# Optimization experiments

Hardware: AMD Instinct MI355X
Metric: run time of the kernel (lower is better)

## Reference

```python
import jax, jax.numpy as jnp
import numpy as np

N = 50000          # nodes
E_RAND = 800000    # random edges (avg degree 16)
IN, HID, HEADS, OUT = 256, 64, 4, 40
NEG_SLOPE = 0.2    # PyG GATConv default leaky_relu slope
BN_EPS = 1e-5


def setup_inputs() -> dict:
    key = jax.random.key(0)
    ks = jax.random.split(key, 24)
    x = jax.random.normal(ks[0], (N, IN), jnp.float32)
    ei = jax.random.randint(ks[1], (2, E_RAND), 0, N)
    loops = jnp.arange(N, dtype=ei.dtype)
    edge_index = jnp.concatenate([ei, jnp.stack([loops, loops])], axis=1)  # add self loops (PyG default)
    s = 0.1
    d = {
        "x": x,
        "edge_index": edge_index,
        "W0": jax.random.normal(ks[2], (IN, HEADS * HID), jnp.float32) * s,
        "a_src0": jax.random.normal(ks[3], (HEADS, HID), jnp.float32) * s,
        "a_dst0": jax.random.normal(ks[4], (HEADS, HID), jnp.float32) * s,
        "b0": jax.random.normal(ks[5], (HEADS * HID,), jnp.float32) * s,
        "bn0_g": jnp.ones((HEADS * HID,), jnp.float32),
        "bn0_b": jnp.zeros((HEADS * HID,), jnp.float32),
        "bn0_m": jax.random.normal(ks[6], (HEADS * HID,), jnp.float32) * s,
        "bn0_v": jax.random.uniform(ks[7], (HEADS * HID,), jnp.float32, 0.5, 1.5),
        "W1": jax.random.normal(ks[8], (HEADS * HID, HEADS * HID), jnp.float32) * s,
        "a_src1": jax.random.normal(ks[9], (HEADS, HID), jnp.float32) * s,
        "a_dst1": jax.random.normal(ks[10], (HEADS, HID), jnp.float32) * s,
        "b1": jax.random.normal(ks[11], (HEADS * HID,), jnp.float32) * s,
        "bn1_g": jnp.ones((HEADS * HID,), jnp.float32),
        "bn1_b": jnp.zeros((HEADS * HID,), jnp.float32),
        "bn1_m": jax.random.normal(ks[12], (HEADS * HID,), jnp.float32) * s,
        "bn1_v": jax.random.uniform(ks[13], (HEADS * HID,), jnp.float32, 0.5, 1.5),
        "W2": jax.random.normal(ks[14], (HEADS * HID, OUT), jnp.float32) * s,
        "a_src2": jax.random.normal(ks[15], (1, OUT), jnp.float32) * s,
        "a_dst2": jax.random.normal(ks[16], (1, OUT), jnp.float32) * s,
        "b2": jax.random.normal(ks[17], (OUT,), jnp.float32) * s,
    }
    return d


def gat_conv(x, edge_index, W, att_src, att_dst, heads, ch):
    """PyG GATConv (eval mode): gather -> leaky_relu attn -> segment softmax -> scatter add."""
    src, dst = edge_index[0], edge_index[1]
    h = (x @ W).reshape(-1, heads, ch)                       # [N,H,C]
    a_s = jnp.einsum('nhc,hc->nh', h, att_src)
    a_d = jnp.einsum('nhc,hc->nh', h, att_dst)
    e = jax.nn.leaky_relu(a_s[src] + a_d[dst], NEG_SLOPE)    # [E,H]
    m = jax.ops.segment_max(e, dst, num_segments=N)
    m = jax.lax.stop_gradient(jnp.where(jnp.isfinite(m), m, 0.0))
    p = jnp.exp(e - m[dst])
    denom = jax.ops.segment_sum(p, dst, num_segments=N)
    alpha = p / (denom[dst] + 1e-16)                         # [E,H]
    msg = h[src] * alpha[:, :, None]                         # [E,H,C]
    return jax.ops.segment_sum(msg, dst, num_segments=N)     # [N,H,C]


def _bn(h, g, b, m, v):
    return g * (h - m) * jax.lax.rsqrt(v + BN_EPS) + b


def reference(x, edge_index, W0, a_src0, a_dst0, b0, bn0_g, bn0_b, bn0_m, bn0_v,
              W1, a_src1, a_dst1, b1, bn1_g, bn1_b, bn1_m, bn1_v,
              W2, a_src2, a_dst2, b2):
    h = gat_conv(x, edge_index, W0, a_src0, a_dst0, HEADS, HID).reshape(N, HEADS * HID) + b0
    h = jax.nn.elu(_bn(h, bn0_g, bn0_b, bn0_m, bn0_v))
    h = gat_conv(h, edge_index, W1, a_src1, a_dst1, HEADS, HID).reshape(N, HEADS * HID) + b1
    h = jax.nn.elu(_bn(h, bn1_g, bn1_b, bn1_m, bn1_v))
    out = gat_conv(h, edge_index, W2, a_src2, a_dst2, 1, OUT).reshape(N, OUT) + b2
    return out
```

## Files before the change

### kernel.cpp

```cpp
#include <hip/hip_runtime.h>
#include <cstdint>
#include <cstddef>

constexpr int kN = 50000;
constexpr float kSlope = 0.2f;
constexpr float kBnEps = 1e-5f;

static inline int ceil_div(int a, int b) { return (a + b - 1) / b; }

typedef __attribute__((ext_vector_type(8))) _Float16 half8;
typedef __attribute__((ext_vector_type(8))) unsigned short ushortx8;
typedef __attribute__((ext_vector_type(4))) float f32x4;

__device__ inline unsigned short f2h_us(float f) {
  _Float16 h = (_Float16)f;
  return *(unsigned short*)&h;
}

__device__ inline void gload16(const void* g, void* l) {
  __builtin_amdgcn_global_load_lds((const __attribute__((address_space(1))) unsigned int*)g,
                                   (__attribute__((address_space(3))) unsigned int*)l, 16, 0, 0);
}


__global__ void k_degree(const int* __restrict__ dst, int* __restrict__ deg, int E) {
  int e = blockIdx.x * blockDim.x + threadIdx.x;
  if (e < E) atomicAdd(&deg[dst[e]], 1);
}

__global__ void k_scan1(const int* __restrict__ deg, int* __restrict__ rp,
                        int* __restrict__ bsum, int n) {
  __shared__ int sm[256];
  int i = blockIdx.x * 256 + threadIdx.x;
  int v = (i < n) ? deg[i] : 0;
  sm[threadIdx.x] = v;
  __syncthreads();
  for (int off = 1; off < 256; off <<= 1) {
    int t = (threadIdx.x >= off) ? sm[threadIdx.x - off] : 0;
    __syncthreads();
    sm[threadIdx.x] += t;
    __syncthreads();
  }
  if (i < n) rp[i + 1] = sm[threadIdx.x];
  if (threadIdx.x == 255) bsum[blockIdx.x] = sm[255];
}

__global__ void k_scan2(int* bsum, int nb) {
  __shared__ int sm[256];
  int v = (threadIdx.x < nb) ? bsum[threadIdx.x] : 0;
  sm[threadIdx.x] = v;
  __syncthreads();
  for (int off = 1; off < 256; off <<= 1) {
    int t = (threadIdx.x >= off) ? sm[threadIdx.x - off] : 0;
    __syncthreads();
    sm[threadIdx.x] += t;
    __syncthreads();
  }
  if (threadIdx.x < nb) bsum[threadIdx.x] = sm[threadIdx.x] - v;
}

__global__ void k_scan3(int* __restrict__ rp, const int* __restrict__ bsum, int n) {
  int i = blockIdx.x * 256 + threadIdx.x;
  if (i < n) rp[i + 1] += bsum[blockIdx.x];
  if (i == 0) rp[0] = 0;
}

__global__ void k_scatter(const int* __restrict__ src, const int* __restrict__ dst,
                          const int* __restrict__ rp, int* __restrict__ cur,
                          int* __restrict__ csr, int E) {
  int e = blockIdx.x * blockDim.x + threadIdx.x;
  if (e < E) {
    int d = dst[e];
    int pos = rp[d] + atomicAdd(&cur[d], 1);
    csr[pos] = src[e];
  }
}


__global__ void k_prep(const float* __restrict__ x, unsigned short* __restrict__ x16,
                       const float* __restrict__ W0, unsigned short* __restrict__ Wt0,
                       const float* __restrict__ W1, unsigned short* __restrict__ Wt1,
                       const float* __restrict__ W2, unsigned short* __restrict__ Wt2) {
  int i = blockIdx.x * blockDim.x + threadIdx.x;
  const int N4 = kN * 64;
  const int S0 = 256 * 256, S1 = 256 * 256, S2 = 128 * 256;
  if (i < N4) {
    float4 v = ((const float4*)x)[i];
    ushort4 o;
    o.x = f2h_us(v.x);
    o.y = f2h_us(v.y);
    o.z = f2h_us(v.z);
    o.w = f2h_us(v.w);
    ((ushort4*)x16)[i] = o;
  } else {
    int j = i - N4;
    if (j < S0) {
      int nc = j >> 8, k = j & 255;
      Wt0[j] = f2h_us(W0[(size_t)k * 256 + nc]);
    } else if (j < S0 + S1) {
      int t = j - S0;
      int nc = t >> 8, k = t & 255;
      Wt1[t] = f2h_us(W1[(size_t)k * 256 + nc]);
    } else if (j < S0 + S1 + S2) {
      int t = j - S0 - S1;
      int nc = t >> 8, k = t & 255;
      Wt2[t] = (nc < 40) ? f2h_us(W2[(size_t)k * 40 + nc]) : (unsigned short)0;
    }
  }
}


__global__ __launch_bounds__(256) void k_mfma_gemm(
    const unsigned short* __restrict__ A, const unsigned short* __restrict__ Bt,
    unsigned short* __restrict__ C, const float* __restrict__ asrc,
    const float* __restrict__ adst, float* __restrict__ a_s, float* __restrict__ a_d, int M,
    int K, int Nc, int ldc, int heads, int acols) {
  constexpr int BM = 128, BK = 32;
  __shared__ unsigned short As[BM * BK];
  __shared__ unsigned short Bs[BM * BK];
  int tid = threadIdx.x;
  int wave = tid >> 6, lane = tid & 63;
  int quad = lane >> 4, l16 = lane & 15;
  int wm = (wave & 1) * 64, wn = (wave >> 1) * 64;
  int bm = blockIdx.x * BM, bn = blockIdx.y * BM;
  int srow = lane >> 2;
  int spart = lane & 3;
  f32x4 acc[4][4] = {};
  for (int k0 = 0; k0 < K; k0 += BK) {
#pragma unroll
    for (int it = 0; it < 2; it++) {
      int chunk = wave * 2 + it;
      int row = chunk * 16 + srow;
      gload16(A + (size_t)(bm + row) * K + k0 + spart * 8, As + chunk * 512);
      gload16(Bt + (size_t)(bn + row) * K + k0 + spart * 8, Bs + chunk * 512);
    }
    __syncthreads();
    half8 af[4], bf[4];
#pragma unroll
    for (int i = 0; i < 4; i++) {
      af[i] = *(const half8*)(As + (wm + i * 16 + l16) * BK + quad * 8);
      bf[i] = *(const half8*)(Bs + (wn + i * 16 + l16) * BK + quad * 8);
    }
#pragma unroll
    for (int i = 0; i < 4; i++)
#pragma unroll
      for (int j = 0; j < 4; j++)
        acc[i][j] = __builtin_amdgcn_mfma_f32_16x16x32_f16(af[i], bf[j], acc[i][j], 0, 0, 0);
    __syncthreads();
  }
#pragma unroll
  for (int i = 0; i < 4; i++) {
#pragma unroll
    for (int j = 0; j < 4; j++) {
      int col = bn + wn + j * 16 + l16;
      if (col >= Nc) continue;
#pragma unroll
      for (int r = 0; r < 4; r++) {
        int row = bm + wm + i * 16 + quad * 4 + r;
        if (row < M) C[(size_t)row * ldc + col] = f2h_us(acc[i][j][r]);
      }
    }
  }
  int ghead = (bn + wn) >> 6;
  if (ghead < heads) {
    float asv[4], adv[4];
#pragma unroll
    for (int j = 0; j < 4; j++) {
      int col = bn + wn + j * 16 + l16;
      bool ok = col < acols;
      asv[j] = ok ? asrc[col] : 0.f;
      adv[j] = ok ? adst[col] : 0.f;
    }
#pragma unroll
    for (int i = 0; i < 4; i++) {
#pragma unroll
      for (int r = 0; r < 4; r++) {
        float s = acc[i][0][r] * asv[0] + acc[i][1][r] * asv[1] + acc[i][2][r] * asv[2] +
                  acc[i][3][r] * asv[3];
        float d = acc[i][0][r] * adv[0] + acc[i][1][r] * adv[1] + acc[i][2][r] * adv[2] +
                  acc[i][3][r] * adv[3];
#pragma unroll
        for (int mask = 1; mask <= 8; mask <<= 1) {
          s += __shfl_xor(s, mask, 64);
          d += __shfl_xor(d, mask, 64);
        }
        if (l16 == 0) {
          int row = bm + wm + i * 16 + quad * 4 + r;
          if (row < M) {
            a_s[row * heads + ghead] = s;
            a_d[row * heads + ghead] = d;
          }
        }
      }
    }
  }
}


__global__ __launch_bounds__(256) void k_attn_agg256(
    const int* __restrict__ rp, const int* __restrict__ csr, const _Float16* __restrict__ h,
    const float* __restrict__ a_s, const float* __restrict__ a_d, const float* __restrict__ bias,
    const float* __restrict__ bg, const float* __restrict__ bb, const float* __restrict__ bm,
    const float* __restrict__ bv, unsigned short* __restrict__ out, int n_nodes) {
  int wid = (blockIdx.x * blockDim.x + threadIdx.x) >> 6;
  int lane = threadIdx.x & 63;
  if (wid >= n_nodes) return;
  int n = wid;
  int beg = rp[n], end = rp[n + 1];
  int half = lane >> 5, l32 = lane & 31;
  int head = l32 >> 3;
  int c = l32 * 8;
  float ad = a_d[n * 4 + head];
  float acc[8] = {};
  float psum = 0.f;
  int e = beg;
  for (; e + 8 <= end; e += 8) {
    int s0 = csr[e + half];
    int s1 = csr[e + 2 + half];
    int s2 = csr[e + 4 + half];
    int s3 = csr[e + 6 + half];
    float x0 = a_s[s0 * 4 + head] + ad;
    float x1 = a_s[s1 * 4 + head] + ad;
    float x2 = a_s[s2 * 4 + head] + ad;
    float x3 = a_s[s3 * 4 + head] + ad;
    half8 v0 = *(const half8*)(h + (size_t)s0 * 256 + c);
    half8 v1 = *(const half8*)(h + (size_t)s1 * 256 + c);
    half8 v2 = *(const half8*)(h + (size_t)s2 * 256 + c);
    half8 v3 = *(const half8*)(h + (size_t)s3 * 256 + c);
    x0 = x0 > 0.f ? x0 : x0 * kSlope;
    x1 = x1 > 0.f ? x1 : x1 * kSlope;
    x2 = x2 > 0.f ? x2 : x2 * kSlope;
    x3 = x3 > 0.f ? x3 : x3 * kSlope;
    float p0 = __expf(x0), p1 = __expf(x1);
    float p2 = __expf(x2), p3 = __expf(x3);
    psum += (p0 + p1) + (p2 + p3);
#pragma unroll
    for (int j = 0; j < 8; j++) {
      acc[j] += (float)v0[j] * p0 + (float)v1[j] * p1;
      acc[j] += (float)v2[j] * p2 + (float)v3[j] * p3;
    }
  }
  for (; e + 2 <= end; e += 2) {
    int s0 = csr[e + half];
    float x0 = a_s[s0 * 4 + head] + ad;
    x0 = x0 > 0.f ? x0 : x0 * kSlope;
    float p0 = __expf(x0);
    psum += p0;
    half8 v0 = *(const half8*)(h + (size_t)s0 * 256 + c);
#pragma unroll
    for (int j = 0; j < 8; j++) acc[j] += (float)v0[j] * p0;
  }
  if (e < end && half == 0) {
    int s0 = csr[e];
    float x0 = a_s[s0 * 4 + head] + ad;
    x0 = x0 > 0.f ? x0 : x0 * kSlope;
    float p0 = __expf(x0);
    psum += p0;
    half8 v0 = *(const half8*)(h + (size_t)s0 * 256 + c);
#pragma unroll
    for (int j = 0; j < 8; j++) acc[j] += (float)v0[j] * p0;
  }
  psum += __shfl_xor(psum, 32, 64);
#pragma unroll
  for (int j = 0; j < 8; j++) acc[j] += __shfl_xor(acc[j], 32, 64);
  if (half == 0) {
    float rden = 1.f / (psum + 1e-16f);
    ushortx8 o;
#pragma unroll
    for (int j = 0; j < 8; j++) {
      float v = acc[j] * rden + bias[c + j];
      v = bg[c + j] * (v - bm[c + j]) * rsqrtf(bv[c + j] + kBnEps) + bb[c + j];
      v = v > 0.f ? v : (__expf(v) - 1.f);
      o[j] = f2h_us(v);
    }
    *(ushortx8*)(out + (size_t)n * 256 + c) = o;
  }
}


__global__ __launch_bounds__(256) void k_attn_agg40(
    const int* __restrict__ rp, const int* __restrict__ csr, const _Float16* __restrict__ h,
    const float* __restrict__ a_s, const float* __restrict__ a_d, const float* __restrict__ bias,
    float* __restrict__ out, int n_nodes) {
  int wid = (blockIdx.x * blockDim.x + threadIdx.x) >> 6;
  int lane = threadIdx.x & 63;
  if (wid >= n_nodes) return;
  int n = wid;
  int beg = rp[n], end = rp[n + 1];
  float ad = a_d[n];
  int grp = lane >> 3, l8 = lane & 7;
  int c = l8 * 8;
  bool act = l8 < 5;
  float acc[8] = {};
  float psum = 0.f;
  for (int base = beg; base < end; base += 16) {
    int e0 = base + grp;
    int e1 = base + 8 + grp;
    if (e0 < end) {
      int s = csr[e0];
      float x = a_s[s] + ad;
      x = x > 0.f ? x : x * kSlope;
      float p = __expf(x);
      psum += p;
      if (act) {
        half8 hv = *(const half8*)(h + (size_t)s * 40 + c);
#pragma unroll
        for (int j = 0; j < 8; j++) acc[j] += (float)hv[j] * p;
      }
    }
    if (e1 < end) {
      int s = csr[e1];
      float x = a_s[s] + ad;
      x = x > 0.f ? x : x * kSlope;
      float p = __expf(x);
      psum += p;
      if (act) {
        half8 hv = *(const half8*)(h + (size_t)s * 40 + c);
#pragma unroll
        for (int j = 0; j < 8; j++) acc[j] += (float)hv[j] * p;
      }
    }
  }
#pragma unroll
  for (int mask = 8; mask <= 32; mask <<= 1) psum += __shfl_xor(psum, mask, 64);
#pragma unroll
  for (int j = 0; j < 8; j++) {
#pragma unroll
    for (int mask = 8; mask <= 32; mask <<= 1) acc[j] += __shfl_xor(acc[j], mask, 64);
  }
  if (lane < 5) {
    float rden = 1.f / (psum + 1e-16f);
    float4 o0, o1;
    o0.x = acc[0] * rden + bias[c + 0];
    o0.y = acc[1] * rden + bias[c + 1];
    o0.z = acc[2] * rden + bias[c + 2];
    o0.w = acc[3] * rden + bias[c + 3];
    o1.x = acc[4] * rden + bias[c + 4];
    o1.y = acc[5] * rden + bias[c + 5];
    o1.z = acc[6] * rden + bias[c + 6];
    o1.w = acc[7] * rden + bias[c + 7];
    *(float4*)(out + (size_t)n * 40 + c) = o0;
    *(float4*)(out + (size_t)n * 40 + c + 4) = o1;
  }
}


extern "C" void kernel_launch(void* const* d_in, const int* in_sizes, int n_in, void* d_out,
                              int out_size, void* d_ws, size_t ws_size, hipStream_t stream) {
  const float* x = (const float*)d_in[0];
  const int* ei = (const int*)d_in[1];
  const float* W0 = (const float*)d_in[2];
  const float* as0 = (const float*)d_in[3];
  const float* ad0 = (const float*)d_in[4];
  const float* b0 = (const float*)d_in[5];
  const float* bg0 = (const float*)d_in[6];
  const float* bb0 = (const float*)d_in[7];
  const float* bm0 = (const float*)d_in[8];
  const float* bv0 = (const float*)d_in[9];
  const float* W1 = (const float*)d_in[10];
  const float* as1 = (const float*)d_in[11];
  const float* ad1 = (const float*)d_in[12];
  const float* b1 = (const float*)d_in[13];
  const float* bg1 = (const float*)d_in[14];
  const float* bb1 = (const float*)d_in[15];
  const float* bm1 = (const float*)d_in[16];
  const float* bv1 = (const float*)d_in[17];
  const float* W2 = (const float*)d_in[18];
  const float* as2 = (const float*)d_in[19];
  const float* ad2 = (const float*)d_in[20];
  const float* b2 = (const float*)d_in[21];
  float* out = (float*)d_out;

  const int E = in_sizes[1] / 2;
  const int* srcIdx = ei;
  const int* dstIdx = ei + E;

  char* p = (char*)d_ws;
  auto alloc = [&](size_t bytes) -> void* {
    void* r = (void*)p;
    p += (bytes + 255) & ~(size_t)255;
    return r;
  };
  int* rp = (int*)alloc((kN + 1) * sizeof(int));
  int* degcur = (int*)alloc((size_t)2 * kN * sizeof(int));
  int* deg = degcur;
  int* cur = degcur + kN;
  int* bsum = (int*)alloc(256 * sizeof(int));
  int* csr = (int*)alloc((size_t)E * sizeof(int));
  float* a_s = (float*)alloc((size_t)kN * 4 * sizeof(float));
  float* a_d = (float*)alloc((size_t)kN * 4 * sizeof(float));
  unsigned short* x16 = (unsigned short*)alloc((size_t)kN * 256 * 2);
  unsigned short* h16 = (unsigned short*)alloc((size_t)kN * 256 * 2);
  unsigned short* act16 = (unsigned short*)alloc((size_t)kN * 256 * 2);
  unsigned short* Wt0 = (unsigned short*)alloc((size_t)256 * 256 * 2);
  unsigned short* Wt1 = (unsigned short*)alloc((size_t)256 * 256 * 2);
  unsigned short* Wt2 = (unsigned short*)alloc((size_t)128 * 256 * 2);

  const int eb = ceil_div(E, 256);
  const int nb = ceil_div(kN, 256);

  hipMemsetAsync(degcur, 0, (size_t)2 * kN * sizeof(int), stream);
  k_degree<<<eb, 256, 0, stream>>>(dstIdx, deg, E);
  k_scan1<<<nb, 256, 0, stream>>>(deg, rp, bsum, kN);
  k_scan2<<<1, 256, 0, stream>>>(bsum, nb);
  k_scan3<<<nb, 256, 0, stream>>>(rp, bsum, kN);
  k_scatter<<<eb, 256, 0, stream>>>(srcIdx, dstIdx, rp, cur, csr, E);

  const int prep_items = kN * 64 + 256 * 256 * 2 + 128 * 256;
  k_prep<<<ceil_div(prep_items, 256), 256, 0, stream>>>(x, x16, W0, Wt0, W1, Wt1, W2, Wt2);

  dim3 gg(ceil_div(kN, 128), 2);
  dim3 gg2(ceil_div(kN, 128), 1);
  int wpn_blocks = ceil_div(kN, 4);

  k_mfma_gemm<<<gg, 256, 0, stream>>>(x16, Wt0, h16, as0, ad0, a_s, a_d, kN, 256, 256, 256, 4,
                                      256);
  k_attn_agg256<<<wpn_blocks, 256, 0, stream>>>(rp, csr, (const _Float16*)h16, a_s, a_d, b0, bg0,
                                                bb0, bm0, bv0, act16, kN);

  k_mfma_gemm<<<gg, 256, 0, stream>>>(act16, Wt1, h16, as1, ad1, a_s, a_d, kN, 256, 256, 256, 4,
                                      256);
  k_attn_agg256<<<wpn_blocks, 256, 0, stream>>>(rp, csr, (const _Float16*)h16, a_s, a_d, b1, bg1,
                                                bb1, bm1, bv1, act16, kN);

  k_mfma_gemm<<<gg2, 256, 0, stream>>>(act16, Wt2, h16, as2, ad2, a_s, a_d, kN, 256, 40, 40, 1,
                                       40);
  k_attn_agg40<<<wpn_blocks, 256, 0, stream>>>(rp, csr, (const _Float16*)h16, a_s, a_d, b2, out,
                                               kN);
}
```

Before: 459.1 us.

## Split 256-wide aggregation into two half-channel blocks with 4 edge lanes per wave

The 256-channel attention aggregation now assigns each node to two blocks, each covering 128 channels. Within a wave, four 16-lane groups each take a different edge, handling eight edges per iteration. The separate unrolled and remainder loops are replaced by one loop that clamps out-of-range edge indices and zeroes their weights. This doubles the number of waves and raises edge-level parallelism per wave, aiming to hide gather latency on low-degree nodes, at the cost of loading each edge's index and attention score twice and doing more cross-lane reduction.

Measured after the change: 472.1 us. 1.03x slower.

```diff
diff --git a/kernel.cpp b/kernel.cpp
--- a/kernel.cpp
+++ b/kernel.cpp
@@ -202,68 +202,47 @@
     const float* __restrict__ a_s, const float* __restrict__ a_d, const float* __restrict__ bias,
     const float* __restrict__ bg, const float* __restrict__ bb, const float* __restrict__ bm,
     const float* __restrict__ bv, unsigned short* __restrict__ out, int n_nodes) {
-  int wid = (blockIdx.x * blockDim.x + threadIdx.x) >> 6;
+  int hf = blockIdx.x & 1;
+  int wave = threadIdx.x >> 6;
   int lane = threadIdx.x & 63;
-  if (wid >= n_nodes) return;
-  int n = wid;
+  int n = (blockIdx.x >> 1) * 4 + wave;
+  if (n >= n_nodes) return;
   int beg = rp[n], end = rp[n + 1];
-  int half = lane >> 5, l32 = lane & 31;
-  int head = l32 >> 3;
-  int c = l32 * 8;
+  int q = lane >> 4, l16 = lane & 15;
+  int c = hf * 128 + l16 * 8;
+  int head = c >> 6;
   float ad = a_d[n * 4 + head];
   float acc[8] = {};
   float psum = 0.f;
-  int e = beg;
-  for (; e + 8 <= end; e += 8) {
-    int s0 = csr[e + half];
-    int s1 = csr[e + 2 + half];
-    int s2 = csr[e + 4 + half];
-    int s3 = csr[e + 6 + half];
-    float x0 = a_s[s0 * 4 + head] + ad;
-    float x1 = a_s[s1 * 4 + head] + ad;
-    float x2 = a_s[s2 * 4 + head] + ad;
-    float x3 = a_s[s3 * 4 + head] + ad;
-    half8 v0 = *(const half8*)(h + (size_t)s0 * 256 + c);
-    half8 v1 = *(const half8*)(h + (size_t)s1 * 256 + c);
-    half8 v2 = *(const half8*)(h + (size_t)s2 * 256 + c);
-    half8 v3 = *(const half8*)(h + (size_t)s3 * 256 + c);
-    x0 = x0 > 0.f ? x0 : x0 * kSlope;
-    x1 = x1 > 0.f ? x1 : x1 * kSlope;
-    x2 = x2 > 0.f ? x2 : x2 * kSlope;
-    x3 = x3 > 0.f ? x3 : x3 * kSlope;
-    float p0 = __expf(x0), p1 = __expf(x1);
-    float p2 = __expf(x2), p3 = __expf(x3);
-    psum += (p0 + p1) + (p2 + p3);
-#pragma unroll
-    for (int j = 0; j < 8; j++) {
-      acc[j] += (float)v0[j] * p0 + (float)v1[j] * p1;
-      acc[j] += (float)v2[j] * p2 + (float)v3[j] * p3;
-    }
-  }
-  for (; e + 2 <= end; e += 2) {
-    int s0 = csr[e + half];
-    float x0 = a_s[s0 * 4 + head] + ad;
-    x0 = x0 > 0.f ? x0 : x0 * kSlope;
-    float p0 = __expf(x0);
-    psum += p0;
-    half8 v0 = *(const half8*)(h + (size_t)s0 * 256 + c);
-#pragma unroll
-    for (int j = 0; j < 8; j++) acc[j] += (float)v0[j] * p0;
-  }
-  if (e < end && half == 0) {
-    int s0 = csr[e];
-    float x0 = a_s[s0 * 4 + head] + ad;
-    x0 = x0 > 0.f ? x0 : x0 * kSlope;
-    float p0 = __expf(x0);
-    psum += p0;
-    half8 v0 = *(const half8*)(h + (size_t)s0 * 256 + c);
-#pragma unroll
-    for (int j = 0; j < 8; j++) acc[j] += (float)v0[j] * p0;
-  }
+  int last = end - 1;
+  for (int e = beg; e < end; e += 8) {
+    int ea = e + q, eb = e + 4 + q;
+    int ia = (ea <= last) ? ea : last;
+    int ib = (eb <= last) ? eb : last;
+    int sa = csr[ia];
+    int sb = csr[ib];
+    float ta = a_s[sa * 4 + head];
+    float tb = a_s[sb * 4 + head];
+    half8 va = *(const half8*)(h + (size_t)sa * 256 + c);
+    half8 vb = *(const half8*)(h + (size_t)sb * 256 + c);
+    float xa = ta + ad, xb = tb + ad;
+    xa = xa > 0.f ? xa : xa * kSlope;
+    xb = xb > 0.f ? xb : xb * kSlope;
+    float pa = __expf(xa), pb = __expf(xb);
+    pa = (ea < end) ? pa : 0.f;
+    pb = (eb < end) ? pb : 0.f;
+    psum += pa + pb;
+#pragma unroll
+    for (int j = 0; j < 8; j++) acc[j] += (float)va[j] * pa + (float)vb[j] * pb;
+  }
+  psum += __shfl_xor(psum, 16, 64);
   psum += __shfl_xor(psum, 32, 64);
 #pragma unroll
-  for (int j = 0; j < 8; j++) acc[j] += __shfl_xor(acc[j], 32, 64);
-  if (half == 0) {
+  for (int j = 0; j < 8; j++) {
+    acc[j] += __shfl_xor(acc[j], 16, 64);
+    acc[j] += __shfl_xor(acc[j], 32, 64);
+  }
+  if (q == 0) {
     float rden = 1.f / (psum + 1e-16f);
     ushortx8 o;
 #pragma unroll
@@ -411,17 +390,18 @@
 
   dim3 gg(ceil_div(kN, 128), 2);
   dim3 gg2(ceil_div(kN, 128), 1);
+  int agg256_blocks = 2 * ceil_div(kN, 4);
   int wpn_blocks = ceil_div(kN, 4);
 
   k_mfma_gemm<<<gg, 256, 0, stream>>>(x16, Wt0, h16, as0, ad0, a_s, a_d, kN, 256, 256, 256, 4,
                                       256);
-  k_attn_agg256<<<wpn_blocks, 256, 0, stream>>>(rp, csr, (const _Float16*)h16, a_s, a_d, b0, bg0,
-                                                bb0, bm0, bv0, act16, kN);
+  k_attn_agg256<<<agg256_blocks, 256, 0, stream>>>(rp, csr, (const _Float16*)h16, a_s, a_d, b0,
+                                                   bg0, bb0, bm0, bv0, act16, kN);
 
   k_mfma_gemm<<<gg, 256, 0, stream>>>(act16, Wt1, h16, as1, ad1, a_s, a_d, kN, 256, 256, 256, 4,
                                       256);
-  k_attn_agg256<<<wpn_blocks, 256, 0, stream>>>(rp, csr, (const _Float16*)h16, a_s, a_d, b1, bg1,
-                                                bb1, bm1, bv1, act16, kN);
+  k_attn_agg256<<<agg256_blocks, 256, 0, stream>>>(rp, csr, (const _Float16*)h16, a_s, a_d, b1,
+                                                   bg1, bb1, bm1, bv1, act16, kN);
 
   k_mfma_gemm<<<gg2, 256, 0, stream>>>(act16, Wt2, h16, as2, ad2, a_s, a_d, kN, 256, 40, 40, 1,
                                        40);
```

## Fuse CSR build, scans and prep into one cooperative kernel

Applied to the files above, without the earlier changes.

Replaces the memset, degree count, three scan kernels, scatter and fp16 prep kernels with a single cooperative kernel of 1024 blocks that uses grid-wide syncs between phases. The aim is to remove several kernel launches and the gaps between them. In exchange each phase runs with a fixed grid-stride loop of limited parallelism, and five grid syncs are added, which may cost more than the launches they replace.

Result: slower. 993.5 us (+116.4%).

```diff
diff --git a/kernel.cpp b/kernel.cpp
--- a/kernel.cpp
+++ b/kernel.cpp
@@ -1,6 +1,9 @@
 #include <hip/hip_runtime.h>
+#include <hip/hip_cooperative_groups.h>
 #include <cstdint>
 #include <cstddef>
+
+namespace cg = cooperative_groups;
 
 constexpr int kN = 50000;
 constexpr float kSlope = 0.2f;
@@ -23,89 +26,100 @@
 }
 
 
-__global__ void k_degree(const int* __restrict__ dst, int* __restrict__ deg, int E) {
-  int e = blockIdx.x * blockDim.x + threadIdx.x;
-  if (e < E) atomicAdd(&deg[dst[e]], 1);
-}
-
-__global__ void k_scan1(const int* __restrict__ deg, int* __restrict__ rp,
-                        int* __restrict__ bsum, int n) {
+__global__ void k_build(const int* __restrict__ src, const int* __restrict__ dst,
+                        int* __restrict__ rp, int* __restrict__ deg, int* __restrict__ cur,
+                        int* __restrict__ bsum, int* __restrict__ csr, int E, int n,
+                        const float* __restrict__ x, unsigned short* __restrict__ x16,
+                        const float* __restrict__ W0, unsigned short* __restrict__ Wt0,
+                        const float* __restrict__ W1, unsigned short* __restrict__ Wt1,
+                        const float* __restrict__ W2, unsigned short* __restrict__ Wt2) {
+  cg::grid_group grid = cg::this_grid();
+  const int tid = blockIdx.x * blockDim.x + threadIdx.x;
+  const int nthr = gridDim.x * blockDim.x;
   __shared__ int sm[256];
-  int i = blockIdx.x * 256 + threadIdx.x;
-  int v = (i < n) ? deg[i] : 0;
-  sm[threadIdx.x] = v;
-  __syncthreads();
-  for (int off = 1; off < 256; off <<= 1) {
-    int t = (threadIdx.x >= off) ? sm[threadIdx.x - off] : 0;
+
+  for (int i = tid; i < n; i += nthr) {
+    deg[i] = 0;
+    cur[i] = 0;
+  }
+  {
+    const int N4 = kN * 64;
+    const int S0 = 256 * 256, S1 = 256 * 256, S2 = 128 * 256;
+    const int total = N4 + S0 + S1 + S2;
+    for (int i = tid; i < total; i += nthr) {
+      if (i < N4) {
+        float4 v = ((const float4*)x)[i];
+        ushort4 o;
+        o.x = f2h_us(v.x);
+        o.y = f2h_us(v.y);
+        o.z = f2h_us(v.z);
+        o.w = f2h_us(v.w);
+        ((ushort4*)x16)[i] = o;
+      } else {
+        int j = i - N4;
+        if (j < S0) {
+          int nc = j >> 8, k = j & 255;
+          Wt0[j] = f2h_us(W0[(size_t)k * 256 + nc]);
+        } else if (j < S0 + S1) {
+          int t = j - S0;
+          int nc = t >> 8, k = t & 255;
+          Wt1[t] = f2h_us(W1[(size_t)k * 256 + nc]);
+        } else {
+          int t = j - S0 - S1;
+          int nc = t >> 8, k = t & 255;
+          Wt2[t] = (nc < 40) ? f2h_us(W2[(size_t)k * 40 + nc]) : (unsigned short)0;
+        }
+      }
+    }
+  }
+  grid.sync();
+
+  for (int e = tid; e < E; e += nthr) atomicAdd(&deg[dst[e]], 1);
+  grid.sync();
+
+  const int nchunks = (n + 255) / 256;
+  for (int c = blockIdx.x; c < nchunks; c += gridDim.x) {
+    int i = c * 256 + threadIdx.x;
+    int v = (i < n) ? deg[i] : 0;
+    sm[threadIdx.x] = v;
     __syncthreads();
-    sm[threadIdx.x] += t;
+    for (int off = 1; off < 256; off <<= 1) {
+      int t = (threadIdx.x >= off) ? sm[threadIdx.x - off] : 0;
+      __syncthreads();
+      sm[threadIdx.x] += t;
+      __syncthreads();
+    }
+    if (i < n) rp[i + 1] = sm[threadIdx.x];
+    if (threadIdx.x == 255) bsum[c] = sm[255];
     __syncthreads();
   }
-  if (i < n) rp[i + 1] = sm[threadIdx.x];
-  if (threadIdx.x == 255) bsum[blockIdx.x] = sm[255];
-}
-
-__global__ void k_scan2(int* bsum, int nb) {
-  __shared__ int sm[256];
-  int v = (threadIdx.x < nb) ? bsum[threadIdx.x] : 0;
-  sm[threadIdx.x] = v;
-  __syncthreads();
-  for (int off = 1; off < 256; off <<= 1) {
-    int t = (threadIdx.x >= off) ? sm[threadIdx.x - off] : 0;
+  grid.sync();
+
+  if (blockIdx.x == 0) {
+    int v = (threadIdx.x < nchunks) ? bsum[threadIdx.x] : 0;
+    sm[threadIdx.x] = v;
     __syncthreads();
-    sm[threadIdx.x] += t;
-    __syncthreads();
-  }
-  if (threadIdx.x < nb) bsum[threadIdx.x] = sm[threadIdx.x] - v;
-}
-
-__global__ void k_scan3(int* __restrict__ rp, const int* __restrict__ bsum, int n) {
-  int i = blockIdx.x * 256 + threadIdx.x;
-  if (i < n) rp[i + 1] += bsum[blockIdx.x];
-  if (i == 0) rp[0] = 0;
-}
-
-__global__ void k_scatter(const int* __restrict__ src, const int* __restrict__ dst,
-                          const int* __restrict__ rp, int* __restrict__ cur,
-                          int* __restrict__ csr, int E) {
-  int e = blockIdx.x * blockDim.x + threadIdx.x;
-  if (e < E) {
+    for (int off = 1; off < 256; off <<= 1) {
+      int t = (threadIdx.x >= off) ? sm[threadIdx.x - off] : 0;
+      __syncthreads();
+      sm[threadIdx.x] += t;
+      __syncthreads();
+    }
+    if (threadIdx.x < nchunks) bsum[threadIdx.x] = sm[threadIdx.x] - v;
+  }
+  grid.sync();
+
+  for (int c = blockIdx.x; c < nchunks; c += gridDim.x) {
+    int i = c * 256 + threadIdx.x;
+    if (i < n) rp[i + 1] += bsum[c];
+  }
+  if (tid == 0) rp[0] = 0;
+  grid.sync();
+
+  for (int e = tid; e < E; e += nthr) {
     int d = dst[e];
     int pos = rp[d] + atomicAdd(&cur[d], 1);
     csr[pos] = src[e];
-  }
-}
-
-
-__global__ void k_prep(const float* __restrict__ x, unsigned short* __restrict__ x16,
-                       const float* __restrict__ W0, unsigned short* __restrict__ Wt0,
-                       const float* __restrict__ W1, unsigned short* __restrict__ Wt1,
-                       const float* __restrict__ W2, unsigned short* __restrict__ Wt2) {
-  int i = blockIdx.x * blockDim.x + threadIdx.x;
-  const int N4 = kN * 64;
-  const int S0 = 256 * 256, S1 = 256 * 256, S2 = 128 * 256;
-  if (i < N4) {
-    float4 v = ((const float4*)x)[i];
-    ushort4 o;
-    o.x = f2h_us(v.x);
-    o.y = f2h_us(v.y);
-    o.z = f2h_us(v.z);
-    o.w = f2h_us(v.w);
-    ((ushort4*)x16)[i] = o;
-  } else {
-    int j = i - N4;
-    if (j < S0) {
-      int nc = j >> 8, k = j & 255;
-      Wt0[j] = f2h_us(W0[(size_t)k * 256 + nc]);
-    } else if (j < S0 + S1) {
-      int t = j - S0;
-      int nc = t >> 8, k = t & 255;
-      Wt1[t] = f2h_us(W1[(size_t)k * 256 + nc]);
-    } else if (j < S0 + S1 + S2) {
-      int t = j - S0 - S1;
-      int nc = t >> 8, k = t & 255;
-      Wt2[t] = (nc < 40) ? f2h_us(W2[(size_t)k * 40 + nc]) : (unsigned short)0;
-    }
   }
 }
 
@@ -396,18 +410,14 @@
   unsigned short* Wt1 = (unsigned short*)alloc((size_t)256 * 256 * 2);
   unsigned short* Wt2 = (unsigned short*)alloc((size_t)128 * 256 * 2);
 
-  const int eb = ceil_div(E, 256);
-  const int nb = ceil_div(kN, 256);
-
-  hipMemsetAsync(degcur, 0, (size_t)2 * kN * sizeof(int), stream);
-  k_degree<<<eb, 256, 0, stream>>>(dstIdx, deg, E);
-  k_scan1<<<nb, 256, 0, stream>>>(deg, rp, bsum, kN);
-  k_scan2<<<1, 256, 0, stream>>>(bsum, nb);
-  k_scan3<<<nb, 256, 0, stream>>>(rp, bsum, kN);
-  k_scatter<<<eb, 256, 0, stream>>>(srcIdx, dstIdx, rp, cur, csr, E);
-
-  const int prep_items = kN * 64 + 256 * 256 * 2 + 128 * 256;
-  k_prep<<<ceil_div(prep_items, 256), 256, 0, stream>>>(x, x16, W0, Wt0, W1, Wt1, W2, Wt2);
+  {
+    int Ee = E, nn = kN;
+    void* args[] = {(void*)&srcIdx, (void*)&dstIdx, (void*)&rp,  (void*)&deg, (void*)&cur,
+                    (void*)&bsum,   (void*)&csr,    (void*)&Ee,  (void*)&nn,  (void*)&x,
+                    (void*)&x16,    (void*)&W0,     (void*)&Wt0, (void*)&W1,  (void*)&Wt1,
+                    (void*)&W2,     (void*)&Wt2};
+    hipLaunchCooperativeKernel((const void*)k_build, dim3(1024), dim3(256), args, 0, stream);
+  }
 
   dim3 gg(ceil_div(kN, 128), 2);
   dim3 gg2(ceil_div(kN, 128), 1);
```

## Fuse degree count with fp16 prep, and CSR scatter with first GEMM

Applied to the files above, without the earlier changes.

Merges the degree-counting kernel with the fp16 conversion/transpose prep into one grid-stride kernel. It also runs the CSR scatter as extra blocks of the layer-0 GEMM launch, since the two are independent. This removes two kernel launches and lets the atomic-heavy scatter overlap the MFMA GEMM. The cost is a mixed-role kernel with GEMM-sized register and LDS use for the scatter blocks, and a fixed 2048-block grid for the prep.

Result: faster. 445.8 us (-2.9%).

```diff
diff --git a/kernel.cpp b/kernel.cpp
--- a/kernel.cpp
+++ b/kernel.cpp
@@ -23,10 +23,44 @@
 }
 
 
-__global__ void k_degree(const int* __restrict__ dst, int* __restrict__ deg, int E) {
-  int e = blockIdx.x * blockDim.x + threadIdx.x;
-  if (e < E) atomicAdd(&deg[dst[e]], 1);
-}
+__global__ void k_prep_degree(const int* __restrict__ dst, int* __restrict__ deg, int E,
+                              const float* __restrict__ x, unsigned short* __restrict__ x16,
+                              const float* __restrict__ W0, unsigned short* __restrict__ Wt0,
+                              const float* __restrict__ W1, unsigned short* __restrict__ Wt1,
+                              const float* __restrict__ W2, unsigned short* __restrict__ Wt2) {
+  const int tid = blockIdx.x * blockDim.x + threadIdx.x;
+  const int nthr = gridDim.x * blockDim.x;
+  for (int e = tid; e < E; e += nthr) atomicAdd(&deg[dst[e]], 1);
+  const int N4 = kN * 64;
+  const int S0 = 256 * 256, S1 = 256 * 256, S2 = 128 * 256;
+  const int total = N4 + S0 + S1 + S2;
+  for (int i = tid; i < total; i += nthr) {
+    if (i < N4) {
+      float4 v = ((const float4*)x)[i];
+      ushort4 o;
+      o.x = f2h_us(v.x);
+      o.y = f2h_us(v.y);
+      o.z = f2h_us(v.z);
+      o.w = f2h_us(v.w);
+      ((ushort4*)x16)[i] = o;
+    } else {
+      int j = i - N4;
+      if (j < S0) {
+        int nc = j >> 8, k = j & 255;
+        Wt0[j] = f2h_us(W0[(size_t)k * 256 + nc]);
+      } else if (j < S0 + S1) {
+        int t = j - S0;
+        int nc = t >> 8, k = t & 255;
+        Wt1[t] = f2h_us(W1[(size_t)k * 256 + nc]);
+      } else {
+        int t = j - S0 - S1;
+        int nc = t >> 8, k = t & 255;
+        Wt2[t] = (nc < 40) ? f2h_us(W2[(size_t)k * 40 + nc]) : (unsigned short)0;
+      }
+    }
+  }
+}
+
 
 __global__ void k_scan1(const int* __restrict__ deg, int* __restrict__ rp,
                         int* __restrict__ bsum, int n) {
@@ -65,53 +99,9 @@
   if (i == 0) rp[0] = 0;
 }
 
-__global__ void k_scatter(const int* __restrict__ src, const int* __restrict__ dst,
-                          const int* __restrict__ rp, int* __restrict__ cur,
-                          int* __restrict__ csr, int E) {
-  int e = blockIdx.x * blockDim.x + threadIdx.x;
-  if (e < E) {
-    int d = dst[e];
-    int pos = rp[d] + atomicAdd(&cur[d], 1);
-    csr[pos] = src[e];
-  }
-}
-
-
-__global__ void k_prep(const float* __restrict__ x, unsigned short* __restrict__ x16,
-                       const float* __restrict__ W0, unsigned short* __restrict__ Wt0,
-                       const float* __restrict__ W1, unsigned short* __restrict__ Wt1,
-                       const float* __restrict__ W2, unsigned short* __restrict__ Wt2) {
-  int i = blockIdx.x * blockDim.x + threadIdx.x;
-  const int N4 = kN * 64;
-  const int S0 = 256 * 256, S1 = 256 * 256, S2 = 128 * 256;
-  if (i < N4) {
-    float4 v = ((const float4*)x)[i];
-    ushort4 o;
-    o.x = f2h_us(v.x);
-    o.y = f2h_us(v.y);
-    o.z = f2h_us(v.z);
-    o.w = f2h_us(v.w);
-    ((ushort4*)x16)[i] = o;
-  } else {
-    int j = i - N4;
-    if (j < S0) {
-      int nc = j >> 8, k = j & 255;
-      Wt0[j] = f2h_us(W0[(size_t)k * 256 + nc]);
-    } else if (j < S0 + S1) {
-      int t = j - S0;
-      int nc = t >> 8, k = t & 255;
-      Wt1[t] = f2h_us(W1[(size_t)k * 256 + nc]);
-    } else if (j < S0 + S1 + S2) {
-      int t = j - S0 - S1;
-      int nc = t >> 8, k = t & 255;
-      Wt2[t] = (nc < 40) ? f2h_us(W2[(size_t)k * 40 + nc]) : (unsigned short)0;
-    }
-  }
-}
-
-
-__global__ __launch_bounds__(256) void k_mfma_gemm(
-    const unsigned short* __restrict__ A, const unsigned short* __restrict__ Bt,
+
+__device__ __forceinline__ void gemm_body(
+    int bx, int by, const unsigned short* __restrict__ A, const unsigned short* __restrict__ Bt,
     unsigned short* __restrict__ C, const float* __restrict__ asrc,
     const float* __restrict__ adst, float* __restrict__ a_s, float* __restrict__ a_d, int M,
     int K, int Nc, int ldc, int heads, int acols) {
@@ -122,7 +112,7 @@
   int wave = tid >> 6, lane = tid & 63;
   int quad = lane >> 4, l16 = lane & 15;
   int wm = (wave & 1) * 64, wn = (wave >> 1) * 64;
-  int bm = blockIdx.x * BM, bn = blockIdx.y * BM;
+  int bm = bx * BM, bn = by * BM;
   int srow = lane >> 2;
   int spart = lane & 3;
   f32x4 acc[4][4] = {};
@@ -192,6 +182,34 @@
           }
         }
       }
+    }
+  }
+}
+
+__global__ __launch_bounds__(256) void k_mfma_gemm(
+    const unsigned short* __restrict__ A, const unsigned short* __restrict__ Bt,
+    unsigned short* __restrict__ C, const float* __restrict__ asrc,
+    const float* __restrict__ adst, float* __restrict__ a_s, float* __restrict__ a_d, int M,
+    int K, int Nc, int ldc, int heads, int acols) {
+  gemm_body(blockIdx.x, blockIdx.y, A, Bt, C, asrc, adst, a_s, a_d, M, K, Nc, ldc, heads, acols);
+}
+
+
+__global__ __launch_bounds__(256) void k_gemm0_scatter(
+    const unsigned short* __restrict__ A, const unsigned short* __restrict__ Bt,
+    unsigned short* __restrict__ C, const float* __restrict__ asrc,
+    const float* __restrict__ adst, float* __restrict__ a_s, float* __restrict__ a_d, int M,
+    int K, int gemmBlocks, const int* __restrict__ src, const int* __restrict__ dst,
+    const int* __restrict__ rp, int* __restrict__ cur, int* __restrict__ csr, int E) {
+  if ((int)blockIdx.x < gemmBlocks) {
+    int bx = blockIdx.x >> 1, by = blockIdx.x & 1;
+    gemm_body(bx, by, A, Bt, C, asrc, adst, a_s, a_d, M, K, 256, 256, 4, 256);
+  } else {
+    int e = (blockIdx.x - gemmBlocks) * 256 + threadIdx.x;
+    if (e < E) {
+      int d = dst[e];
+      int pos = rp[d] + atomicAdd(&cur[d], 1);
+      csr[pos] = src[e];
     }
   }
 }
@@ -396,25 +414,23 @@
   unsigned short* Wt1 = (unsigned short*)alloc((size_t)256 * 256 * 2);
   unsigned short* Wt2 = (unsigned short*)alloc((size_t)128 * 256 * 2);
 
-  const int eb = ceil_div(E, 256);
   const int nb = ceil_div(kN, 256);
+  const int sblocks = ceil_div(E, 256);
 
   hipMemsetAsync(degcur, 0, (size_t)2 * kN * sizeof(int), stream);
-  k_degree<<<eb, 256, 0, stream>>>(dstIdx, deg, E);
+  k_prep_degree<<<2048, 256, 0, stream>>>(dstIdx, deg, E, x, x16, W0, Wt0, W1, Wt1, W2, Wt2);
   k_scan1<<<nb, 256, 0, stream>>>(deg, rp, bsum, kN);
   k_scan2<<<1, 256, 0, stream>>>(bsum, nb);
   k_scan3<<<nb, 256, 0, stream>>>(rp, bsum, kN);
-  k_scatter<<<eb, 256, 0, stream>>>(srcIdx, dstIdx, rp, cur, csr, E);
-
-  const int prep_items = kN * 64 + 256 * 256 * 2 + 128 * 256;
-  k_prep<<<ceil_div(prep_items, 256), 256, 0, stream>>>(x, x16, W0, Wt0, W1, Wt1, W2, Wt2);
+
+  const int gemmBlocks = ceil_div(kN, 128) * 2;
+  k_gemm0_scatter<<<gemmBlocks + sblocks, 256, 0, stream>>>(
+      x16, Wt0, h16, as0, ad0, a_s, a_d, kN, 256, gemmBlocks, srcIdx, dstIdx, rp, cur, csr, E);
 
   dim3 gg(ceil_div(kN, 128), 2);
   dim3 gg2(ceil_div(kN, 128), 1);
   int wpn_blocks = ceil_div(kN, 4);
 
-  k_mfma_gemm<<<gg, 256, 0, stream>>>(x16, Wt0, h16, as0, ad0, a_s, a_d, kN, 256, 256, 256, 4,
-                                      256);
   k_attn_agg256<<<wpn_blocks, 256, 0, stream>>>(rp, csr, (const _Float16*)h16, a_s, a_d, b0, bg0,
                                                 bb0, bm0, bv0, act16, kN);
 
```
